# Kernel optimization log

Measured on AMD Instinct MI355X. Metric: run time of the kernel, lower is better.

Reference implementation:

```python
import jax, jax.numpy as jnp
import numpy as np

L1 = 1536
L2 = 15
L3 = 64
COUNT = 8
B = 16384


def setup_inputs() -> dict:
    key = jax.random.key(0)
    ks = jax.random.split(key, 10)
    d_in = 2 * L1 // 2  # 1536
    s1 = 1.0 / np.sqrt(d_in)
    s2 = 1.0 / np.sqrt(2 * L2)
    s3 = 1.0 / np.sqrt(L3)
    return {
        "x": jax.random.normal(ks[0], (B, d_in), dtype=jnp.float32),
        "ls_indices": jax.random.randint(ks[1], (B,), 0, COUNT, dtype=jnp.int32),
        "W1": jax.random.uniform(ks[2], (COUNT * (L2 + 1), d_in), jnp.float32, -s1, s1),
        "b1": jax.random.uniform(ks[3], (COUNT * (L2 + 1),), jnp.float32, -s1, s1),
        "Wf": jax.random.uniform(ks[4], (L2 + 1, d_in), jnp.float32, -s1, s1),
        "bf": jax.random.uniform(ks[5], (L2 + 1,), jnp.float32, -s1, s1),
        "W2": jax.random.uniform(ks[6], (COUNT * L3, 2 * L2), jnp.float32, -s2, s2),
        "b2": jax.random.uniform(ks[7], (COUNT * L3,), jnp.float32, -s2, s2),
        "Wo": jax.random.uniform(ks[8], (COUNT, L3), jnp.float32, -s3, s3),
        "bo": jax.random.uniform(ks[9], (COUNT,), jnp.float32, -s3, s3),
    }


def reference(x, ls_indices, W1, b1, Wf, bf, W2, b2, Wo, bo):
    count = Wo.shape[0]
    n = x.shape[0]
    idx = ls_indices[:, None, None]  # [B,1,1] selects the per-sample stack

    # l1: all stacks, then gather selected stack row per sample
    l1s = (x @ W1.T + b1).reshape(n, count, L2 + 1)          # [B, count, 16]
    l1f = x @ Wf.T + bf                                       # [B, 16]
    l1c = jnp.take_along_axis(l1s, idx, axis=1)[:, 0]         # [B, 16]

    l1c_, l1c_out = l1c[:, :L2], l1c[:, L2:]                  # [B,15], [B,1]
    l1f_, l1f_out = l1f[:, :L2], l1f[:, L2:]
    l1x = l1c_ + l1f_
    # squared-clipped-ReLU concat: [pow(x,2)*127/128, x] clamped to [0,1]
    l1x = jnp.clip(jnp.concatenate([l1x * l1x * (127.0 / 128.0), l1x], axis=1), 0.0, 1.0)  # [B,30]

    l2s = (l1x @ W2.T + b2).reshape(n, count, L3)             # [B, count, 64]
    l2c = jnp.take_along_axis(l2s, idx, axis=1)[:, 0]         # [B, 64]
    l2x = jnp.clip(l2c, 0.0, 1.0)

    l3s = (l2x @ Wo.T + bo).reshape(n, count, 1)              # [B, count, 1]
    l3c = jnp.take_along_axis(l3s, idx, axis=1)[:, 0]         # [B, 1]
    return l3c + l1f_out + l1c_out
```

## Files before the change

kernel.cpp:

```cpp
#include <hip/hip_runtime.h>
#include <hip/hip_bf16.h>
#include <stdint.h>

#define L1DIM 1536
#define NOUT  144
#define MTILE 32
#define BK    64
#define NITER (L1DIM / BK)
#define BCH   18

typedef __bf16 bf16;
typedef __bf16 bf16x8 __attribute__((ext_vector_type(8)));
typedef float  floatx4 __attribute__((ext_vector_type(4)));

__global__ void pack_weights(const float* __restrict__ W1,
                             const float* __restrict__ Wf,
                             bf16* __restrict__ pw) {
    int t = blockIdx.x * blockDim.x + threadIdx.x;
    if (t >= NOUT * 192) return;
    int n = t / 192;
    int o = t % 192;
    const float* src = (n < 128) ? (W1 + (size_t)n * L1DIM + o * 8)
                                 : (Wf + (size_t)(n - 128) * L1DIM + o * 8);
    float4 s0 = ((const float4*)src)[0];
    float4 s1 = ((const float4*)src)[1];
    bf16x8 v;
    v[0] = (bf16)s0.x; v[1] = (bf16)s0.y; v[2] = (bf16)s0.z; v[3] = (bf16)s0.w;
    v[4] = (bf16)s1.x; v[5] = (bf16)s1.y; v[6] = (bf16)s1.z; v[7] = (bf16)s1.w;
    *(bf16x8*)(pw + ((size_t)o * NOUT + n) * 8) = v;
}

__device__ __forceinline__ void gload_lds16(const void* g, void* l) {
    __builtin_amdgcn_global_load_lds(
        (const __attribute__((address_space(1))) void*)g,
        (__attribute__((address_space(3))) void*)l, 16, 0, 0);
}

__device__ __forceinline__ bf16x8 cvt8(float4 a, float4 b) {
    bf16x8 r;
    r[0] = (bf16)a.x; r[1] = (bf16)a.y; r[2] = (bf16)a.z; r[3] = (bf16)a.w;
    r[4] = (bf16)b.x; r[5] = (bf16)b.y; r[6] = (bf16)b.z; r[7] = (bf16)b.w;
    return r;
}

__global__ __launch_bounds__(256, 2) void layerstacks_main(
    const float* __restrict__ x, const int* __restrict__ lsidx,
    const bf16* __restrict__ pw,
    const float* __restrict__ b1, const float* __restrict__ bf_,
    const float* __restrict__ W2, const float* __restrict__ b2,
    const float* __restrict__ Wo, const float* __restrict__ bo,
    float* __restrict__ out)
{
    __shared__ float la[2][MTILE * BK];
    __shared__ bf16  lb[2][8 * NOUT * 8];
    __shared__ float ep[MTILE][33];

    const int tid  = threadIdx.x;
    const int wv   = tid >> 6;
    const int ln   = tid & 63;
    const int quad = ln >> 4;
    const int lm   = ln & 15;

    const int R0  = blockIdx.x * MTILE;
    const int ms  = wv & 1;
    const int nh  = wv >> 1;
    const int nt0 = nh ? 5 : 0;
    const int ntn = nh ? 4 : 5;

    const int sr  = ln >> 4;
    const int sch = ln & 15;

    floatx4 acc[5];
#pragma unroll
    for (int i = 0; i < 5; i++) acc[i] = (floatx4){0.f, 0.f, 0.f, 0.f};

#define STAGE(buf, ki_)                                                          \
    {                                                                            \
        const int k0_ = (ki_) * BK;                                              \
        _Pragma("unroll")                                                        \
        for (int jj = 0; jj < 2; jj++) {                                         \
            const int j    = 2 * wv + jj;                                        \
            const int row  = 4 * j + sr;                                         \
            const int cg   = sch ^ (row & 7);                                    \
            gload_lds16(x + (size_t)(R0 + row) * L1DIM + k0_ + cg * 4,           \
                        &la[buf][j * 4 * BK + sr * BK + sch * 4]);               \
        }                                                                        \
        const bf16* bsrc_ = pw + (size_t)(ki_) * 8 * NOUT * 8;                   \
        _Pragma("unroll")                                                        \
        for (int cc = wv; cc < BCH; cc += 4) {                                   \
            gload_lds16(bsrc_ + (size_t)cc * 512 + ln * 8,                       \
                        &lb[buf][(size_t)cc * 512 + ln * 8]);                    \
        }                                                                        \
    }

    STAGE(0, 0)
    __syncthreads();

    for (int ki = 0; ki < NITER; ki++) {
        const int cur = ki & 1;
        if (ki < NITER - 1) STAGE(cur ^ 1, ki + 1)

#pragma unroll
        for (int s = 0; s < 2; s++) {
            const int row = ms * 16 + lm;
            const int c0  = s * 8 + quad * 2;
            float4 a0 = *(const float4*)&la[cur][row * BK + ((c0)     ^ (row & 7)) * 4];
            float4 a1 = *(const float4*)&la[cur][row * BK + ((c0 + 1) ^ (row & 7)) * 4];
            bf16x8 af = cvt8(a0, a1);
            const bf16* bbase = &lb[cur][((size_t)(s * 4 + quad) * NOUT) * 8];
#pragma unroll
            for (int t = 0; t < 5; t++) {
                if (t < ntn) {
                    bf16x8 bfrag = *(const bf16x8*)&bbase[((nt0 + t) * 16 + lm) * 8];
                    acc[t] = __builtin_amdgcn_mfma_f32_16x16x32_bf16(af, bfrag, acc[t], 0, 0, 0);
                }
            }
        }
        __syncthreads();
    }

    {
        const int rbase = ms * 16 + quad * 4;
#pragma unroll
        for (int r = 0; r < 4; r++) {
            const int row = rbase + r;
            const int bkt = lsidx[R0 + row];
            if (nh == 0) {
                float c = acc[0][r];
#pragma unroll
                for (int t = 1; t < 5; t++) c = (bkt == t) ? acc[t][r] : c;
                if (bkt < 5) ep[row][lm] = c;
            } else {
                float c = acc[0][r];
                c = (bkt == 6) ? acc[1][r] : c;
                c = (bkt == 7) ? acc[2][r] : c;
                if (bkt >= 5) ep[row][lm] = c;
                ep[row][16 + lm] = acc[3][r];
            }
        }
    }
    __syncthreads();

    const int er   = tid >> 3;
    const int sub  = tid & 7;
    const int grow = R0 + er;
    const int bkt  = lsidx[grow];

    const float l1c15 = ep[er][15] + b1[bkt * 16 + 15];
    const float l1f15 = ep[er][31] + bf_[15];

    float l1x[30];
#pragma unroll
    for (int j = 0; j < 15; j++) {
        float tj = (ep[er][j] + b1[bkt * 16 + j]) + (ep[er][16 + j] + bf_[j]);
        float sq = tj * tj * (127.0f / 128.0f);
        l1x[j]      = fminf(fmaxf(sq, 0.f), 1.f);
        l1x[15 + j] = fminf(fmaxf(tj, 0.f), 1.f);
    }

    float part = 0.f;
#pragma unroll
    for (int o = 0; o < 8; o++) {
        const int oi = bkt * 64 + sub * 8 + o;
        const float2* wrow = (const float2*)(W2 + oi * 30);
        float a = b2[oi];
#pragma unroll
        for (int j2 = 0; j2 < 15; j2++) {
            float2 w = wrow[j2];
            a += l1x[2 * j2] * w.x + l1x[2 * j2 + 1] * w.y;
        }
        a = fminf(fmaxf(a, 0.f), 1.f);
        part += a * Wo[oi];
    }
    part += __shfl_xor(part, 1);
    part += __shfl_xor(part, 2);
    part += __shfl_xor(part, 4);
    if (sub == 0) out[grow] = part + bo[bkt] + l1c15 + l1f15;
}

extern "C" void kernel_launch(void* const* d_in, const int* in_sizes, int n_in,
                              void* d_out, int out_size, void* d_ws, size_t ws_size,
                              hipStream_t stream) {
    const float* x   = (const float*)d_in[0];
    const int*   idx = (const int*)  d_in[1];
    const float* W1  = (const float*)d_in[2];
    const float* b1  = (const float*)d_in[3];
    const float* Wf  = (const float*)d_in[4];
    const float* bf  = (const float*)d_in[5];
    const float* W2  = (const float*)d_in[6];
    const float* b2  = (const float*)d_in[7];
    const float* Wo  = (const float*)d_in[8];
    const float* bo  = (const float*)d_in[9];
    float* out = (float*)d_out;
    bf16*  pw  = (bf16*)d_ws;

    pack_weights<<<dim3((NOUT * 192 + 255) / 256), dim3(256), 0, stream>>>(W1, Wf, pw);
    layerstacks_main<<<dim3(16384 / MTILE), dim3(256), 0, stream>>>(
        x, idx, pw, b1, bf, W2, b2, Wo, bo, out);
}
```

Measured before the change: 179.5 us.

## Split K across waves with 16-row tiles and direct global B-fragment loads

The row tile shrinks to 16 and BK grows to 128. Each of the four waves now covers a different K slice for all 144 output columns instead of splitting M and N, and the partial sums are reduced through shared memory before the epilogue. Weight fragments are read straight from global memory (through the cache) rather than staged into LDS, which frees LDS and allows higher occupancy (launch bounds 4) and twice as many blocks. The cost is more per-block reduction work, twice as many weight reads from L2, and an epilogue that runs on only half the threads.

```diff
diff --git a/kernel.cpp b/kernel.cpp
--- a/kernel.cpp
+++ b/kernel.cpp
@@ -4,10 +4,9 @@
 
 #define L1DIM 1536
 #define NOUT  144
-#define MTILE 32
-#define BK    64
+#define MTILE 16
+#define BK    128
 #define NITER (L1DIM / BK)
-#define BCH   18
 
 typedef __bf16 bf16;
 typedef __bf16 bf16x8 __attribute__((ext_vector_type(8)));
@@ -43,7 +42,7 @@
     return r;
 }
 
-__global__ __launch_bounds__(256, 2) void layerstacks_main(
+__global__ __launch_bounds__(256, 4) void layerstacks_main(
     const float* __restrict__ x, const int* __restrict__ lsidx,
     const bf16* __restrict__ pw,
     const float* __restrict__ b1, const float* __restrict__ bf_,
@@ -52,130 +51,123 @@
     float* __restrict__ out)
 {
     __shared__ float la[2][MTILE * BK];
-    __shared__ bf16  lb[2][8 * NOUT * 8];
-    __shared__ float ep[MTILE][33];
+    __shared__ float ep4[4][MTILE][33];
 
     const int tid  = threadIdx.x;
     const int wv   = tid >> 6;
     const int ln   = tid & 63;
     const int quad = ln >> 4;
     const int lm   = ln & 15;
+    const int ks   = wv;
 
-    const int R0  = blockIdx.x * MTILE;
-    const int ms  = wv & 1;
-    const int nh  = wv >> 1;
-    const int nt0 = nh ? 5 : 0;
-    const int ntn = nh ? 4 : 5;
+    const int R0 = blockIdx.x * MTILE;
 
-    const int sr  = ln >> 4;
-    const int sch = ln & 15;
+    const int sro = ln >> 5;
+    const int sch = ln & 31;
 
-    floatx4 acc[5];
+    floatx4 acc[9];
 #pragma unroll
-    for (int i = 0; i < 5; i++) acc[i] = (floatx4){0.f, 0.f, 0.f, 0.f};
+    for (int i = 0; i < 9; i++) acc[i] = (floatx4){0.f, 0.f, 0.f, 0.f};
 
-#define STAGE(buf, ki_)                                                          \
-    {                                                                            \
-        const int k0_ = (ki_) * BK;                                              \
-        _Pragma("unroll")                                                        \
-        for (int jj = 0; jj < 2; jj++) {                                         \
-            const int j    = 2 * wv + jj;                                        \
-            const int row  = 4 * j + sr;                                         \
-            const int cg   = sch ^ (row & 7);                                    \
-            gload_lds16(x + (size_t)(R0 + row) * L1DIM + k0_ + cg * 4,           \
-                        &la[buf][j * 4 * BK + sr * BK + sch * 4]);               \
-        }                                                                        \
-        const bf16* bsrc_ = pw + (size_t)(ki_) * 8 * NOUT * 8;                   \
-        _Pragma("unroll")                                                        \
-        for (int cc = wv; cc < BCH; cc += 4) {                                   \
-            gload_lds16(bsrc_ + (size_t)cc * 512 + ln * 8,                       \
-                        &lb[buf][(size_t)cc * 512 + ln * 8]);                    \
-        }                                                                        \
+#define STAGE(buf, ki_)                                                        \
+    {                                                                          \
+        const int k0_ = (ki_) * BK;                                            \
+        _Pragma("unroll")                                                      \
+        for (int jj = 0; jj < 2; jj++) {                                       \
+            const int j   = 2 * wv + jj;                                       \
+            const int row = 2 * j + sro;                                       \
+            const int cg  = sch ^ (row & 7);                                   \
+            gload_lds16(x + (size_t)(R0 + row) * L1DIM + k0_ + cg * 4,         \
+                        &la[buf][j * 2 * BK + sro * BK + sch * 4]);            \
+        }                                                                      \
     }
 
     STAGE(0, 0)
     __syncthreads();
 
+    const int c0 = ks * 8 + quad * 2;
+
     for (int ki = 0; ki < NITER; ki++) {
         const int cur = ki & 1;
         if (ki < NITER - 1) STAGE(cur ^ 1, ki + 1)
 
+        const int row = lm;
+        float4 a0 = *(const float4*)&la[cur][row * BK + ((c0)     ^ (row & 7)) * 4];
+        float4 a1 = *(const float4*)&la[cur][row * BK + ((c0 + 1) ^ (row & 7)) * 4];
+        bf16x8 af = cvt8(a0, a1);
+
+        const bf16* bsl = pw + ((size_t)(ki * 16 + ks * 4 + quad) * NOUT) * 8;
 #pragma unroll
-        for (int s = 0; s < 2; s++) {
-            const int row = ms * 16 + lm;
-            const int c0  = s * 8 + quad * 2;
-            float4 a0 = *(const float4*)&la[cur][row * BK + ((c0)     ^ (row & 7)) * 4];
-            float4 a1 = *(const float4*)&la[cur][row * BK + ((c0 + 1) ^ (row & 7)) * 4];
-            bf16x8 af = cvt8(a0, a1);
-            const bf16* bbase = &lb[cur][((size_t)(s * 4 + quad) * NOUT) * 8];
-#pragma unroll
-            for (int t = 0; t < 5; t++) {
-                if (t < ntn) {
-                    bf16x8 bfrag = *(const bf16x8*)&bbase[((nt0 + t) * 16 + lm) * 8];
-                    acc[t] = __builtin_amdgcn_mfma_f32_16x16x32_bf16(af, bfrag, acc[t], 0, 0, 0);
-                }
-            }
+        for (int t = 0; t < 9; t++) {
+            bf16x8 bfrag = *(const bf16x8*)(bsl + ((size_t)(t * 16 + lm)) * 8);
+            acc[t] = __builtin_amdgcn_mfma_f32_16x16x32_bf16(af, bfrag, acc[t], 0, 0, 0);
         }
         __syncthreads();
     }
 
     {
-        const int rbase = ms * 16 + quad * 4;
 #pragma unroll
         for (int r = 0; r < 4; r++) {
-            const int row = rbase + r;
+            const int row = quad * 4 + r;
             const int bkt = lsidx[R0 + row];
-            if (nh == 0) {
-                float c = acc[0][r];
+            float c = acc[0][r];
 #pragma unroll
-                for (int t = 1; t < 5; t++) c = (bkt == t) ? acc[t][r] : c;
-                if (bkt < 5) ep[row][lm] = c;
-            } else {
-                float c = acc[0][r];
-                c = (bkt == 6) ? acc[1][r] : c;
-                c = (bkt == 7) ? acc[2][r] : c;
-                if (bkt >= 5) ep[row][lm] = c;
-                ep[row][16 + lm] = acc[3][r];
-            }
+            for (int t = 1; t < 8; t++) c = (bkt == t) ? acc[t][r] : c;
+            ep4[ks][row][lm]      = c;
+            ep4[ks][row][16 + lm] = acc[8][r];
         }
     }
     __syncthreads();
 
-    const int er   = tid >> 3;
-    const int sub  = tid & 7;
-    const int grow = R0 + er;
-    const int bkt  = lsidx[grow];
+    {
+        const int col = tid & 31;
+        const int rr  = tid >> 5;
+#pragma unroll
+        for (int p = 0; p < 2; p++) {
+            const int row = rr + p * 8;
+            ep4[0][row][col] = ep4[0][row][col] + ep4[1][row][col]
+                             + ep4[2][row][col] + ep4[3][row][col];
+        }
+    }
+    __syncthreads();
 
-    const float l1c15 = ep[er][15] + b1[bkt * 16 + 15];
-    const float l1f15 = ep[er][31] + bf_[15];
+    if (tid < 128) {
+        const int er   = tid >> 3;
+        const int sub  = tid & 7;
+        const int grow = R0 + er;
+        const int bkt  = lsidx[grow];
 
-    float l1x[30];
+        const float l1c15 = ep4[0][er][15] + b1[bkt * 16 + 15];
+        const float l1f15 = ep4[0][er][31] + bf_[15];
+
+        float l1x[30];
 #pragma unroll
-    for (int j = 0; j < 15; j++) {
-        float tj = (ep[er][j] + b1[bkt * 16 + j]) + (ep[er][16 + j] + bf_[j]);
-        float sq = tj * tj * (127.0f / 128.0f);
-        l1x[j]      = fminf(fmaxf(sq, 0.f), 1.f);
-        l1x[15 + j] = fminf(fmaxf(tj, 0.f), 1.f);
+        for (int j = 0; j < 15; j++) {
+            float tj = (ep4[0][er][j] + b1[bkt * 16 + j]) + (ep4[0][er][16 + j] + bf_[j]);
+            float sq = tj * tj * (127.0f / 128.0f);
+            l1x[j]      = fminf(fmaxf(sq, 0.f), 1.f);
+            l1x[15 + j] = fminf(fmaxf(tj, 0.f), 1.f);
+        }
+
+        float part = 0.f;
+#pragma unroll
+        for (int o = 0; o < 8; o++) {
+            const int oi = bkt * 64 + sub * 8 + o;
+            const float2* wrow = (const float2*)(W2 + oi * 30);
+            float a = b2[oi];
+#pragma unroll
+            for (int j2 = 0; j2 < 15; j2++) {
+                float2 w = wrow[j2];
+                a += l1x[2 * j2] * w.x + l1x[2 * j2 + 1] * w.y;
+            }
+            a = fminf(fmaxf(a, 0.f), 1.f);
+            part += a * Wo[oi];
+        }
+        part += __shfl_xor(part, 1);
+        part += __shfl_xor(part, 2);
+        part += __shfl_xor(part, 4);
+        if (sub == 0) out[grow] = part + bo[bkt] + l1c15 + l1f15;
     }
-
-    float part = 0.f;
-#pragma unroll
-    for (int o = 0; o < 8; o++) {
-        const int oi = bkt * 64 + sub * 8 + o;
-        const float2* wrow = (const float2*)(W2 + oi * 30);
-        float a = b2[oi];
-#pragma unroll
-        for (int j2 = 0; j2 < 15; j2++) {
-            float2 w = wrow[j2];
-            a += l1x[2 * j2] * w.x + l1x[2 * j2 + 1] * w.y;
-        }
-        a = fminf(fmaxf(a, 0.f), 1.f);
-        part += a * Wo[oi];
-    }
-    part += __shfl_xor(part, 1);
-    part += __shfl_xor(part, 2);
-    part += __shfl_xor(part, 4);
-    if (sub == 0) out[grow] = part + bo[bkt] + l1c15 + l1f15;
 }
 
 extern "C" void kernel_launch(void* const* d_in, const int* in_sizes, int n_in,
```

Result: no change. 182.0 us (+1.4%).
